# Optimization experiments

Hardware: AMD Instinct MI355X
Metric: run time of the kernel (lower is better)

The kernel has to match this reference:

```python
import jax, jax.numpy as jnp
import numpy as np

D_MODEL = 2048
N_HEADS = 16
HEAD_DIM = 128
ROPE_THETA = 10000.0


def _rope_cache(seq_len, dim, theta):
    inv_freq = 1.0 / (theta ** (jnp.arange(0, dim, 2, dtype=jnp.float32) / dim))
    t = jnp.arange(seq_len, dtype=jnp.float32)
    freqs = jnp.outer(t, inv_freq)          # [T, dim/2]
    emb = jnp.concatenate([freqs, freqs], axis=-1)  # [T, dim]
    return jnp.cos(emb), jnp.sin(emb)


def _rotate_half(x):
    d = x.shape[-1] // 2
    return jnp.concatenate([-x[..., d:], x[..., :d]], axis=-1)


def setup_inputs() -> dict:
    key = jax.random.key(0)
    k1, k2, k3 = jax.random.split(key, 3)
    B, T, D = 2, 2048, D_MODEL
    x = jax.random.normal(k1, (B, T, D), dtype=jnp.float32)
    w_qkv = jax.random.normal(k2, (D, 3 * D), dtype=jnp.float32) * (D ** -0.5)
    w_out = jax.random.normal(k3, (D, D), dtype=jnp.float32) * (D ** -0.5)
    return {"x": x, "w_qkv": w_qkv, "w_out": w_out}


def reference(x, w_qkv, w_out):
    B, T, D = x.shape
    H, Hd = N_HEADS, HEAD_DIM
    qkv = x @ w_qkv                                  # [B, T, 3D]
    q, k, v = jnp.split(qkv, 3, axis=-1)
    # [B, H, T, Hd]
    q = q.reshape(B, T, H, Hd).transpose(0, 2, 1, 3)
    k = k.reshape(B, T, H, Hd).transpose(0, 2, 1, 3)
    v = v.reshape(B, T, H, Hd).transpose(0, 2, 1, 3)
    cos, sin = _rope_cache(T, Hd, ROPE_THETA)        # [T, Hd]
    cos = cos[None, None]                            # [1,1,T,Hd]
    sin = sin[None, None]
    q = q * cos + _rotate_half(q) * sin
    k = k * cos + _rotate_half(k) * sin
    scale = Hd ** -0.5
    logits = jnp.einsum('bhqd,bhkd->bhqk', q, k) * scale
    causal = jnp.tril(jnp.ones((T, T), dtype=bool))
    logits = jnp.where(causal[None, None], logits, jnp.finfo(logits.dtype).min)
    attn = jax.nn.softmax(logits, axis=-1)
    out = jnp.einsum('bhqk,bhkd->bhqd', attn, v)     # [B,H,T,Hd]
    out = out.transpose(0, 2, 1, 3).reshape(B, T, D)
    return out @ w_out
```

## Files before the change

kernel.cpp:

```cpp
#include <hip/hip_runtime.h>

typedef unsigned short u16;
typedef unsigned int u32;
typedef __bf16 bf16x8 __attribute__((ext_vector_type(8)));
typedef float f32x4 __attribute__((ext_vector_type(4)));
typedef u16 u16x8 __attribute__((ext_vector_type(8)));

#define T_SEQ 2048
#define DMODEL 2048
#define NQKV 6144
#define HD 128
#define NH 16
#define MROWS 4096

__device__ __forceinline__ u16 f2b(float f) {
  union { float f; u32 u; } a; a.f = f;
  u32 r = a.u + 0x7fffu + ((a.u >> 16) & 1u);
  return (u16)(r >> 16);
}
__device__ __forceinline__ float b2f(u16 h) {
  union { u32 u; float f; } a; a.u = ((u32)h) << 16;
  return a.f;
}
__device__ __forceinline__ void g2l16(const u16* g, u16* l) {
  __builtin_amdgcn_global_load_lds((const __attribute__((address_space(1))) u32*)g,
                                   (__attribute__((address_space(3))) u32*)l, 16, 0, 0);
}

__global__ void k_f32_to_bf16(const float* __restrict__ in, u16* __restrict__ out, int n) {
  int i = (blockIdx.x * 256 + threadIdx.x) * 8;
  if (i >= n) return;
  float4 a = *(const float4*)(in + i);
  float4 b = *(const float4*)(in + i + 4);
  u16x8 v;
  v[0] = f2b(a.x); v[1] = f2b(a.y); v[2] = f2b(a.z); v[3] = f2b(a.w);
  v[4] = f2b(b.x); v[5] = f2b(b.y); v[6] = f2b(b.z); v[7] = f2b(b.w);
  *(u16x8*)(out + i) = v;
}

__global__ void k_transpose_bf16(const float* __restrict__ in, u16* __restrict__ out,
                                 int R, int C) {
  __shared__ u16 tile[32][33];
  const int c0 = blockIdx.x * 32, r0 = blockIdx.y * 32;
  const int tx = threadIdx.x & 31, ty = threadIdx.x >> 5;
#pragma unroll
  for (int i = 0; i < 32; i += 8)
    tile[ty + i][tx] = f2b(in[(size_t)(r0 + ty + i) * C + c0 + tx]);
  __syncthreads();
#pragma unroll
  for (int i = 0; i < 32; i += 8)
    out[(size_t)(c0 + ty + i) * R + r0 + tx] = tile[tx][ty + i];
}

__global__ void k_rope_cache(float* __restrict__ cosb, float* __restrict__ sinb) {
  int idx = blockIdx.x * 256 + threadIdx.x;
  int t = idx >> 6, d = idx & 63;
  float inv = powf(10000.0f, -(float)d * (1.0f / 64.0f));
  float fr = (float)t * inv;
  cosb[idx] = cosf(fr);
  sinb[idx] = sinf(fr);
}

template <int EPI>
__global__ __launch_bounds__(256) void k_gemm_nt(const u16* __restrict__ A,
                                                 const u16* __restrict__ B,
                                                 void* __restrict__ Cv,
                                                 int M, int N, int K) {
  __shared__ __align__(16) u16 lA[128 * 64];
  __shared__ __align__(16) u16 lB[128 * 64];
  const int tid = threadIdx.x;
  const int wid = tid >> 6, lane = tid & 63;
  const int g = lane >> 4, q = lane & 15;
  const int wr = wid >> 1, wc = wid & 1;
  const int bn = blockIdx.x, bm = blockIdx.y;
  const int l8 = lane >> 3, l7 = lane & 7;
  const f32x4 fzero = {0.f, 0.f, 0.f, 0.f};
  f32x4 acc[4][4];
#pragma unroll
  for (int m = 0; m < 4; ++m)
#pragma unroll
    for (int n = 0; n < 4; ++n) acc[m][n] = fzero;

  const u16* Ab = A + (size_t)bm * 128 * K;
  const u16* Bb = B + (size_t)bn * 128 * K;

  for (int k0 = 0; k0 < K; k0 += 64) {
    __syncthreads();
#pragma unroll
    for (int i = 0; i < 4; ++i) {
      int chunk = wid * 4 + i;
      int row = chunk * 8 + l8;
      int scol = (l7 * 8) ^ ((row & 7) << 3);
      g2l16(Ab + (size_t)row * K + k0 + scol, lA + chunk * 512);
      g2l16(Bb + (size_t)row * K + k0 + scol, lB + chunk * 512);
    }
    __syncthreads();
#pragma unroll
    for (int kk = 0; kk < 2; ++kk) {
      bf16x8 af[4], bfr[4];
#pragma unroll
      for (int m = 0; m < 4; ++m) {
        int row = wr * 64 + m * 16 + q;
        int col = (kk * 32 + g * 8) ^ ((row & 7) << 3);
        af[m] = *(const bf16x8*)(lA + row * 64 + col);
      }
#pragma unroll
      for (int n = 0; n < 4; ++n) {
        int row = wc * 64 + n * 16 + q;
        int col = (kk * 32 + g * 8) ^ ((row & 7) << 3);
        bfr[n] = *(const bf16x8*)(lB + row * 64 + col);
      }
#pragma unroll
      for (int m = 0; m < 4; ++m)
#pragma unroll
        for (int n = 0; n < 4; ++n)
          acc[m][n] = __builtin_amdgcn_mfma_f32_16x16x32_bf16(af[m], bfr[n], acc[m][n], 0, 0, 0);
    }
  }
  const int rbase = bm * 128 + wr * 64;
  const int cbase = bn * 128 + wc * 64;
#pragma unroll
  for (int m = 0; m < 4; ++m)
#pragma unroll
    for (int n = 0; n < 4; ++n) {
      int col = cbase + n * 16 + q;
#pragma unroll
      for (int r = 0; r < 4; ++r) {
        int row = rbase + m * 16 + g * 4 + r;
        if (EPI == 0)
          ((u16*)Cv)[(size_t)row * N + col] = f2b(acc[m][n][r]);
        else
          ((float*)Cv)[(size_t)row * N + col] = acc[m][n][r];
      }
    }
}

__global__ __launch_bounds__(256) void k_scatter_rope(const u16* __restrict__ qkv,
                                                      const float* __restrict__ cosb,
                                                      const float* __restrict__ sinb,
                                                      u16* __restrict__ qr,
                                                      u16* __restrict__ kr,
                                                      u16* __restrict__ vtb) {
  __shared__ __align__(16) u16 vtile[128][72];
  const int bh = blockIdx.x, b = bh >> 4, h = bh & 15;
  const int t0 = blockIdx.y * 64;
  const int tid = threadIdx.x;
  const float qscale = 0.08838834764831845f;
#pragma unroll
  for (int which = 0; which < 2; ++which) {
    u16* dst = which ? kr : qr;
    const int colbase = which * DMODEL + h * HD;
    const float sc = which ? 1.0f : qscale;
    for (int i = 0; i < 4; ++i) {
      int c = i * 256 + tid;
      int tt = c >> 4, d0 = (c & 15) * 8;
      int t = t0 + tt;
      size_t rowoff = (size_t)(b * T_SEQ + t) * NQKV + colbase;
      u16x8 xa = *(const u16x8*)(qkv + rowoff + d0);
      u16x8 xpart = *(const u16x8*)(qkv + rowoff + (d0 ^ 64));
      int dm = d0 & 63;
      bool lowhalf = d0 < 64;
      u16x8 y;
#pragma unroll
      for (int j = 0; j < 8; ++j) {
        float cv = cosb[t * 64 + dm + j];
        float sv = sinb[t * 64 + dm + j];
        float x0 = b2f(xa[j]), x1 = b2f(xpart[j]);
        float yv = lowhalf ? (x0 * cv - x1 * sv) : (x0 * cv + x1 * sv);
        y[j] = f2b(yv * sc);
      }
      *(u16x8*)(dst + ((size_t)bh * T_SEQ + t) * HD + d0) = y;
    }
  }
  for (int i = 0; i < 4; ++i) {
    int c = i * 256 + tid;
    int tt = c >> 4, d0 = (c & 15) * 8;
    size_t rowoff = (size_t)(b * T_SEQ + t0 + tt) * NQKV + 2 * DMODEL + h * HD;
    u16x8 xv = *(const u16x8*)(qkv + rowoff + d0);
#pragma unroll
    for (int j = 0; j < 8; ++j) vtile[d0 + j][tt] = xv[j];
  }
  __syncthreads();
  for (int i = 0; i < 4; ++i) {
    int c = i * 256 + tid;
    int d = c >> 3, tc = (c & 7) * 8;
    u16x8 y = *(const u16x8*)(&vtile[d][tc]);
    *(u16x8*)(vtb + ((size_t)bh * HD + d) * T_SEQ + t0 + tc) = y;
  }
}

__global__ __launch_bounds__(256) void k_attn(const u16* __restrict__ qr,
                                              const u16* __restrict__ kr,
                                              const u16* __restrict__ vtb,
                                              u16* __restrict__ ao) {
  __shared__ __align__(16) u16 lK[64 * 128];
  __shared__ __align__(16) u16 lV[128 * 64];
  __shared__ __align__(16) u16 lP[4][16 * 72];
  const int bh = blockIdx.x, b = bh >> 4, h = bh & 15;
  const int qt = blockIdx.y;
  const int tid = threadIdx.x;
  const int wid = tid >> 6, lane = tid & 63;
  const int g = lane >> 4, q = lane & 15;
  const int qw0 = qt * 64 + wid * 16;
  const u16* qb = qr + (size_t)bh * T_SEQ * HD;
  const u16* kbp = kr + (size_t)bh * T_SEQ * HD;
  const u16* vb = vtb + (size_t)bh * HD * T_SEQ;
  const f32x4 fzero = {0.f, 0.f, 0.f, 0.f};

  bf16x8 qf[4];
#pragma unroll
  for (int ks = 0; ks < 4; ++ks)
    qf[ks] = *(const bf16x8*)(qb + (size_t)(qw0 + q) * HD + ks * 32 + g * 8);

  f32x4 o_acc[8];
#pragma unroll
  for (int n = 0; n < 8; ++n) o_acc[n] = fzero;
  float m_run = -1e30f, l_run = 0.f;

  const int ntiles = qt + 1;
  for (int kt = 0; kt < ntiles; ++kt) {
    const int kb = kt * 64;
    __syncthreads();
#pragma unroll
    for (int i = 0; i < 4; ++i) {
      int chunk = wid * 4 + i;
      int row = chunk * 4 + g;
      int scol = (q * 8) ^ ((row & 7) << 3);
      g2l16(kbp + (size_t)(kb + row) * HD + scol, lK + chunk * 512);
    }
#pragma unroll
    for (int i = 0; i < 4; ++i) {
      int chunk = wid * 4 + i;
      int row = chunk * 8 + (lane >> 3);
      int scol = ((lane & 7) * 8) ^ ((row & 7) << 3);
      g2l16(vb + (size_t)row * T_SEQ + kb + scol, lV + chunk * 512);
    }
    __syncthreads();
    {
      f32x4 st[4];
#pragma unroll
      for (int m = 0; m < 4; ++m) st[m] = fzero;
#pragma unroll
      for (int ks = 0; ks < 4; ++ks) {
#pragma unroll
        for (int m = 0; m < 4; ++m) {
          int row = m * 16 + q;
          int col = (ks * 32 + g * 8) ^ ((row & 7) << 3);
          bf16x8 kf = *(const bf16x8*)(lK + row * 128 + col);
          st[m] = __builtin_amdgcn_mfma_f32_16x16x32_bf16(kf, qf[ks], st[m], 0, 0, 0);
        }
      }
      const int qrow = qw0 + q;
      float p[4][4];
      float pmax = -1e30f;
#pragma unroll
      for (int m = 0; m < 4; ++m)
#pragma unroll
        for (int r = 0; r < 4; ++r) {
          int kcol = kb + m * 16 + g * 4 + r;
          float s = (kcol <= qrow) ? st[m][r] : -1e30f;
          p[m][r] = s;
          pmax = fmaxf(pmax, s);
        }
      pmax = fmaxf(pmax, __shfl_xor(pmax, 16));
      pmax = fmaxf(pmax, __shfl_xor(pmax, 32));
      float m_new = fmaxf(m_run, pmax);
      float corr = __expf(m_run - m_new);
      float ls = 0.f;
#pragma unroll
      for (int m = 0; m < 4; ++m)
#pragma unroll
        for (int r = 0; r < 4; ++r) {
          float e = __expf(p[m][r] - m_new);
          p[m][r] = e;
          ls += e;
        }
      ls += __shfl_xor(ls, 16);
      ls += __shfl_xor(ls, 32);
      l_run = l_run * corr + ls;
      m_run = m_new;
#pragma unroll
      for (int m = 0; m < 4; ++m) {
#pragma unroll
        for (int rp = 0; rp < 2; ++rp) {
          u32 pk = (u32)f2b(p[m][rp * 2]) | ((u32)f2b(p[m][rp * 2 + 1]) << 16);
          *(u32*)(&lP[wid][q * 72 + m * 16 + g * 4 + rp * 2]) = pk;
        }
      }
      asm volatile("s_waitcnt lgkmcnt(0)" ::: "memory");
      __builtin_amdgcn_sched_barrier(0);
      float corr4[4];
#pragma unroll
      for (int r = 0; r < 4; ++r) corr4[r] = __shfl(corr, g * 4 + r);
#pragma unroll
      for (int n = 0; n < 8; ++n) {
#pragma unroll
        for (int r = 0; r < 4; ++r) o_acc[n][r] *= corr4[r];
      }
#pragma unroll
      for (int ks = 0; ks < 2; ++ks) {
        bf16x8 pf = *(const bf16x8*)(&lP[wid][q * 72 + ks * 32 + g * 8]);
#pragma unroll
        for (int n = 0; n < 8; ++n) {
          int row = n * 16 + q;
          int col = (ks * 32 + g * 8) ^ ((row & 7) << 3);
          bf16x8 vf = *(const bf16x8*)(lV + row * 64 + col);
          o_acc[n] = __builtin_amdgcn_mfma_f32_16x16x32_bf16(pf, vf, o_acc[n], 0, 0, 0);
        }
      }
    }
  }
  float linv[4];
#pragma unroll
  for (int r = 0; r < 4; ++r) {
    float lv = __shfl(l_run, g * 4 + r);
    linv[r] = 1.0f / lv;
  }
#pragma unroll
  for (int n = 0; n < 8; ++n)
#pragma unroll
    for (int r = 0; r < 4; ++r) {
      int trow = qw0 + g * 4 + r;
      ao[(size_t)(b * T_SEQ + trow) * DMODEL + h * HD + n * 16 + q] = f2b(o_acc[n][r] * linv[r]);
    }
}

extern "C" void kernel_launch(void* const* d_in, const int* in_sizes, int n_in,
                              void* d_out, int out_size, void* d_ws, size_t ws_size,
                              hipStream_t stream) {
  const float* x = (const float*)d_in[0];
  const float* w_qkv = (const float*)d_in[1];
  const float* w_out = (const float*)d_in[2];
  char* ws = (char*)d_ws;
  size_t off = 0;
  u16* xb = (u16*)(ws + off);    off += (size_t)MROWS * DMODEL * 2;
  u16* wqkvT = (u16*)(ws + off); off += (size_t)NQKV * DMODEL * 2;
  u16* woutT = (u16*)(ws + off); off += (size_t)DMODEL * DMODEL * 2;
  u16* qkv = (u16*)(ws + off);   off += (size_t)MROWS * NQKV * 2;
  u16* qr = (u16*)(ws + off);    off += (size_t)32 * T_SEQ * HD * 2;
  u16* kr = (u16*)(ws + off);    off += (size_t)32 * T_SEQ * HD * 2;
  u16* vtb = (u16*)(ws + off);   off += (size_t)32 * T_SEQ * HD * 2;
  float* cosb = (float*)(ws + off); off += (size_t)T_SEQ * 64 * 4;
  float* sinb = (float*)(ws + off); off += (size_t)T_SEQ * 64 * 4;
  u16* ao = xb;

  k_f32_to_bf16<<<dim3(MROWS * DMODEL / (256 * 8)), 256, 0, stream>>>(x, xb, MROWS * DMODEL);
  k_transpose_bf16<<<dim3(NQKV / 32, DMODEL / 32), 256, 0, stream>>>(w_qkv, wqkvT, DMODEL, NQKV);
  k_transpose_bf16<<<dim3(DMODEL / 32, DMODEL / 32), 256, 0, stream>>>(w_out, woutT, DMODEL, DMODEL);
  k_rope_cache<<<dim3(T_SEQ * 64 / 256), 256, 0, stream>>>(cosb, sinb);
  k_gemm_nt<0><<<dim3(NQKV / 128, MROWS / 128), 256, 0, stream>>>(xb, wqkvT, qkv, MROWS, NQKV, DMODEL);
  k_scatter_rope<<<dim3(32, T_SEQ / 64), 256, 0, stream>>>(qkv, cosb, sinb, qr, kr, vtb);
  k_attn<<<dim3(32, T_SEQ / 64), 256, 0, stream>>>(qr, kr, vtb, ao);
  k_gemm_nt<1><<<dim3(DMODEL / 128, MROWS / 128), 256, 0, stream>>>(ao, woutT, d_out, MROWS, DMODEL, DMODEL);
}
```

Before: 300.2 us.

## Replace GEMM with 8-wave 256-row tiled kernel using quarter-tile pipelined staging

Replaces the simple 128x128 single-buffered GEMM with an 8-wave (512-thread) kernel on 256xBN tiles. The kernel double-buffers LDS, splits each tile into half-tiles and interleaves async global-to-LDS loads for later k-tiles with MFMA phases, using explicit vmcnt waits, barriers and setprio. The goal is to hide global memory latency and raise arithmetic intensity for both the QKV and output projections. In exchange it uses more LDS, more registers and more complex synchronisation, and the larger tiles produce fewer blocks for the smaller output GEMM.

```diff
diff --git a/kernel.cpp b/kernel.cpp
--- a/kernel.cpp
+++ b/kernel.cpp
@@ -26,6 +26,8 @@
   __builtin_amdgcn_global_load_lds((const __attribute__((address_space(1))) u32*)g,
                                    (__attribute__((address_space(3))) u32*)l, 16, 0, 0);
 }
+
+#define BAR() do { asm volatile("" ::: "memory"); __builtin_amdgcn_s_barrier(); asm volatile("" ::: "memory"); } while (0)
 
 __global__ void k_f32_to_bf16(const float* __restrict__ in, u16* __restrict__ out, int n) {
   int i = (blockIdx.x * 256 + threadIdx.x) * 8;
@@ -61,78 +63,141 @@
   sinb[idx] = sinf(fr);
 }
 
-template <int EPI>
-__global__ __launch_bounds__(256) void k_gemm_nt(const u16* __restrict__ A,
-                                                 const u16* __restrict__ B,
-                                                 void* __restrict__ Cv,
-                                                 int M, int N, int K) {
-  __shared__ __align__(16) u16 lA[128 * 64];
-  __shared__ __align__(16) u16 lB[128 * 64];
+template <int BN, int EPI>
+__global__ __launch_bounds__(512, 2) void k_gemm8(const u16* __restrict__ A,
+                                                  const u16* __restrict__ B,
+                                                  void* __restrict__ Cv,
+                                                  int M, int N, int K) {
+  constexpr int HN = BN / 2;
+  constexpr int CW = BN / 8;
+  constexpr int FN = CW / 16;
+  constexpr int LB = (HN * 64 * 2) / (512 * 16);
+  constexpr int VM = LB + 2;
+
+  __shared__ __align__(16) u16 lA[2][2][128 * 64];
+  __shared__ __align__(16) u16 lB[2][2][HN * 64];
+
   const int tid = threadIdx.x;
   const int wid = tid >> 6, lane = tid & 63;
   const int g = lane >> 4, q = lane & 15;
-  const int wr = wid >> 1, wc = wid & 1;
-  const int bn = blockIdx.x, bm = blockIdx.y;
+  const int wm = wid >> 2, wn = wid & 3;
   const int l8 = lane >> 3, l7 = lane & 7;
+  const int bmBase = blockIdx.y * 256;
+  const int bnBase = blockIdx.x * BN;
+  const int NT = K >> 6;
+
   const f32x4 fzero = {0.f, 0.f, 0.f, 0.f};
-  f32x4 acc[4][4];
-#pragma unroll
-  for (int m = 0; m < 4; ++m)
-#pragma unroll
-    for (int n = 0; n < 4; ++n) acc[m][n] = fzero;
-
-  const u16* Ab = A + (size_t)bm * 128 * K;
-  const u16* Bb = B + (size_t)bn * 128 * K;
-
-  for (int k0 = 0; k0 < K; k0 += 64) {
-    __syncthreads();
-#pragma unroll
-    for (int i = 0; i < 4; ++i) {
-      int chunk = wid * 4 + i;
-      int row = chunk * 8 + l8;
-      int scol = (l7 * 8) ^ ((row & 7) << 3);
-      g2l16(Ab + (size_t)row * K + k0 + scol, lA + chunk * 512);
-      g2l16(Bb + (size_t)row * K + k0 + scol, lB + chunk * 512);
-    }
-    __syncthreads();
-#pragma unroll
-    for (int kk = 0; kk < 2; ++kk) {
-      bf16x8 af[4], bfr[4];
-#pragma unroll
-      for (int m = 0; m < 4; ++m) {
-        int row = wr * 64 + m * 16 + q;
-        int col = (kk * 32 + g * 8) ^ ((row & 7) << 3);
-        af[m] = *(const bf16x8*)(lA + row * 64 + col);
-      }
-#pragma unroll
-      for (int n = 0; n < 4; ++n) {
-        int row = wc * 64 + n * 16 + q;
-        int col = (kk * 32 + g * 8) ^ ((row & 7) << 3);
-        bfr[n] = *(const bf16x8*)(lB + row * 64 + col);
-      }
-#pragma unroll
-      for (int m = 0; m < 4; ++m)
-#pragma unroll
-        for (int n = 0; n < 4; ++n)
-          acc[m][n] = __builtin_amdgcn_mfma_f32_16x16x32_bf16(af[m], bfr[n], acc[m][n], 0, 0, 0);
-    }
-  }
-  const int rbase = bm * 128 + wr * 64;
-  const int cbase = bn * 128 + wc * 64;
-#pragma unroll
-  for (int m = 0; m < 4; ++m)
-#pragma unroll
-    for (int n = 0; n < 4; ++n) {
-      int col = cbase + n * 16 + q;
-#pragma unroll
-      for (int r = 0; r < 4; ++r) {
-        int row = rbase + m * 16 + g * 4 + r;
-        if (EPI == 0)
-          ((u16*)Cv)[(size_t)row * N + col] = f2b(acc[m][n][r]);
-        else
-          ((float*)Cv)[(size_t)row * N + col] = acc[m][n][r];
-      }
-    }
+  f32x4 acc[2][2][4][FN];
+#pragma unroll
+  for (int ha = 0; ha < 2; ++ha)
+#pragma unroll
+    for (int hb = 0; hb < 2; ++hb)
+#pragma unroll
+      for (int fm = 0; fm < 4; ++fm)
+#pragma unroll
+        for (int fn = 0; fn < FN; ++fn) acc[ha][hb][fm][fn] = fzero;
+
+  auto stageA = [&](int tile, int half, int bufI) {
+    if (tile < NT) {
+#pragma unroll
+      for (int j = 0; j < 2; ++j) {
+        int ch = wid * 2 + j;
+        int r = ch * 8 + l8;
+        int sc = (l7 * 8) ^ ((r & 7) << 3);
+        g2l16(A + (size_t)(bmBase + half * 128 + r) * K + (size_t)tile * 64 + sc,
+              &lA[bufI][half][ch * 512]);
+      }
+    }
+  };
+  auto stageB = [&](int tile, int half, int bufI) {
+    if (tile < NT) {
+#pragma unroll
+      for (int j = 0; j < LB; ++j) {
+        int ch = wid * LB + j;
+        int r = ch * 8 + l8;
+        int sc = (l7 * 8) ^ ((r & 7) << 3);
+        g2l16(B + (size_t)(bnBase + half * HN + r) * K + (size_t)tile * 64 + sc,
+              &lB[bufI][half][ch * 512]);
+      }
+    }
+  };
+
+  stageB(0, 0, 0); stageA(0, 1, 0); stageB(0, 1, 0); stageA(0, 0, 0);
+  stageB(1, 0, 1); stageA(1, 1, 1);
+  if constexpr (VM == 4) asm volatile("s_waitcnt vmcnt(4)" ::: "memory");
+  else                   asm volatile("s_waitcnt vmcnt(3)" ::: "memory");
+  BAR();
+
+#define PHASE(HA, HB, STAGE_STMT, WAIT_STMT)                                         \
+  do {                                                                               \
+    bf16x8 af[4][2];                                                                 \
+    bf16x8 bfr[FN][2];                                                               \
+    _Pragma("unroll") for (int fm = 0; fm < 4; ++fm) {                               \
+      int r = wm * 64 + fm * 16 + q;                                                 \
+      _Pragma("unroll") for (int kk = 0; kk < 2; ++kk) {                             \
+        int c = (kk * 32 + g * 8) ^ ((r & 7) << 3);                                  \
+        af[fm][kk] = *(const bf16x8*)&lA[buf][HA][r * 64 + c];                       \
+      }                                                                              \
+    }                                                                                \
+    _Pragma("unroll") for (int fn = 0; fn < FN; ++fn) {                              \
+      int r = wn * CW + fn * 16 + q;                                                 \
+      _Pragma("unroll") for (int kk = 0; kk < 2; ++kk) {                             \
+        int c = (kk * 32 + g * 8) ^ ((r & 7) << 3);                                  \
+        bfr[fn][kk] = *(const bf16x8*)&lB[buf][HB][r * 64 + c];                      \
+      }                                                                              \
+    }                                                                                \
+    STAGE_STMT;                                                                      \
+    WAIT_STMT;                                                                       \
+    BAR();                                                                           \
+    asm volatile("s_waitcnt lgkmcnt(0)" ::: "memory");                               \
+    __builtin_amdgcn_sched_barrier(0);                                               \
+    __builtin_amdgcn_s_setprio(1);                                                   \
+    _Pragma("unroll") for (int fm = 0; fm < 4; ++fm)                                 \
+      _Pragma("unroll") for (int fn = 0; fn < FN; ++fn) {                            \
+        acc[HA][HB][fm][fn] = __builtin_amdgcn_mfma_f32_16x16x32_bf16(               \
+            af[fm][0], bfr[fn][0], acc[HA][HB][fm][fn], 0, 0, 0);                    \
+        acc[HA][HB][fm][fn] = __builtin_amdgcn_mfma_f32_16x16x32_bf16(               \
+            af[fm][1], bfr[fn][1], acc[HA][HB][fm][fn], 0, 0, 0);                    \
+      }                                                                              \
+    __builtin_amdgcn_s_setprio(0);                                                   \
+    asm volatile("" ::: "memory");                                                   \
+    __builtin_amdgcn_s_barrier();                                                    \
+    asm volatile("" ::: "memory");                                                   \
+  } while (0)
+
+  for (int t = 0; t < NT; ++t) {
+    const int buf = t & 1;
+    PHASE(0, 0, stageB(t + 1, 1, buf ^ 1), );
+    PHASE(1, 0, stageA(t + 1, 0, buf ^ 1), );
+    PHASE(1, 1, stageB(t + 2, 0, buf), );
+    PHASE(0, 1, stageA(t + 2, 1, buf),
+          if (t + 2 < NT) {
+            if constexpr (VM == 4) asm volatile("s_waitcnt vmcnt(4)" ::: "memory");
+            else                   asm volatile("s_waitcnt vmcnt(3)" ::: "memory");
+          } else {
+            asm volatile("s_waitcnt vmcnt(0)" ::: "memory");
+          });
+  }
+#undef PHASE
+
+#pragma unroll
+  for (int ha = 0; ha < 2; ++ha)
+#pragma unroll
+    for (int hb = 0; hb < 2; ++hb)
+#pragma unroll
+      for (int fm = 0; fm < 4; ++fm)
+#pragma unroll
+        for (int fn = 0; fn < FN; ++fn) {
+          int col = bnBase + hb * HN + wn * CW + fn * 16 + q;
+#pragma unroll
+          for (int r = 0; r < 4; ++r) {
+            int row = bmBase + ha * 128 + wm * 64 + fm * 16 + g * 4 + r;
+            if (EPI == 0)
+              ((u16*)Cv)[(size_t)row * N + col] = f2b(acc[ha][hb][fm][fn][r]);
+            else
+              ((float*)Cv)[(size_t)row * N + col] = acc[ha][hb][fm][fn][r];
+          }
+        }
 }
 
 __global__ __launch_bounds__(256) void k_scatter_rope(const u16* __restrict__ qkv,
@@ -348,8 +413,8 @@
   k_transpose_bf16<<<dim3(NQKV / 32, DMODEL / 32), 256, 0, stream>>>(w_qkv, wqkvT, DMODEL, NQKV);
   k_transpose_bf16<<<dim3(DMODEL / 32, DMODEL / 32), 256, 0, stream>>>(w_out, woutT, DMODEL, DMODEL);
   k_rope_cache<<<dim3(T_SEQ * 64 / 256), 256, 0, stream>>>(cosb, sinb);
-  k_gemm_nt<0><<<dim3(NQKV / 128, MROWS / 128), 256, 0, stream>>>(xb, wqkvT, qkv, MROWS, NQKV, DMODEL);
+  k_gemm8<256, 0><<<dim3(NQKV / 256, MROWS / 256), 512, 0, stream>>>(xb, wqkvT, qkv, MROWS, NQKV, DMODEL);
   k_scatter_rope<<<dim3(32, T_SEQ / 64), 256, 0, stream>>>(qkv, cosb, sinb, qr, kr, vtb);
   k_attn<<<dim3(32, T_SEQ / 64), 256, 0, stream>>>(qr, kr, vtb, ao);
-  k_gemm_nt<1><<<dim3(DMODEL / 128, MROWS / 128), 256, 0, stream>>>(ao, woutT, d_out, MROWS, DMODEL, DMODEL);
-}
+  k_gemm8<128, 1><<<dim3(DMODEL / 128, MROWS / 256), 512, 0, stream>>>(ao, woutT, d_out, MROWS, DMODEL, DMODEL);
+}
```

Result: slower. 327.8 us (+9.2%).

## Use 256x256 eight-wave pipelined GEMM for QKV and reverse attention tile order

Applied to the files above, without the earlier changes.

Adds a new QKV projection GEMM with 512 threads and a 256x256 output tile. It uses double-buffered, XOR-swizzled LDS quadrants loaded via global_load_lds and interleaves staging, barriers and MFMA phases with raised priority. This aims to raise reuse and overlap memory with compute. Attention blocks now process query tiles in reverse order, so the longest causal tiles launch first for better load balance. The cost is heavy LDS use (128KB) and a fragile schedule built on waitcnt and barriers.

```diff
diff --git a/kernel.cpp b/kernel.cpp
--- a/kernel.cpp
+++ b/kernel.cpp
@@ -26,6 +26,8 @@
   __builtin_amdgcn_global_load_lds((const __attribute__((address_space(1))) u32*)g,
                                    (__attribute__((address_space(3))) u32*)l, 16, 0, 0);
 }
+
+#define BAR() do { asm volatile("" ::: "memory"); __builtin_amdgcn_s_barrier(); asm volatile("" ::: "memory"); } while (0)
 
 __global__ void k_f32_to_bf16(const float* __restrict__ in, u16* __restrict__ out, int n) {
   int i = (blockIdx.x * 256 + threadIdx.x) * 8;
@@ -59,6 +61,144 @@
   float fr = (float)t * inv;
   cosb[idx] = cosf(fr);
   sinb[idx] = sinf(fr);
+}
+
+template <int EPI>
+__global__ __launch_bounds__(512, 2) void k_gemm8(const u16* __restrict__ A,
+                                                  const u16* __restrict__ B,
+                                                  void* __restrict__ Cv,
+                                                  int M, int N, int K) {
+  __shared__ __align__(16) u16 lA[2][2][128 * 64];
+  __shared__ __align__(16) u16 lB[2][2][128 * 64];
+
+  const int tid = threadIdx.x;
+  const int wid = tid >> 6, lane = tid & 63;
+  const int g = lane >> 4, q = lane & 15;
+  const int wm = wid >> 2, wn = wid & 3;
+  const int l8 = lane >> 3, l7 = lane & 7;
+  const int bmBase = blockIdx.y * 256;
+  const int bnBase = blockIdx.x * 256;
+  const int NT = K >> 6;
+
+  const f32x4 fzero = {0.f, 0.f, 0.f, 0.f};
+  f32x4 acc[2][2][4][2];
+#pragma unroll
+  for (int ha = 0; ha < 2; ++ha)
+#pragma unroll
+    for (int hb = 0; hb < 2; ++hb)
+#pragma unroll
+      for (int fm = 0; fm < 4; ++fm)
+#pragma unroll
+        for (int fn = 0; fn < 2; ++fn) acc[ha][hb][fm][fn] = fzero;
+
+  auto stageA = [&](int tile, int half, int bufI) {
+    if (tile < NT) {
+#pragma unroll
+      for (int j = 0; j < 2; ++j) {
+        int ch = wid * 2 + j;
+        int r = ch * 8 + l8;
+        int sc = (l7 * 8) ^ ((r & 7) << 3);
+        g2l16(A + (size_t)(bmBase + half * 128 + r) * K + (size_t)tile * 64 + sc,
+              &lA[bufI][half][ch * 512]);
+      }
+    }
+  };
+  auto stageB = [&](int tile, int half, int bufI) {
+    if (tile < NT) {
+#pragma unroll
+      for (int j = 0; j < 2; ++j) {
+        int ch = wid * 2 + j;
+        int r = ch * 8 + l8;
+        int sc = (l7 * 8) ^ ((r & 7) << 3);
+        g2l16(B + (size_t)(bnBase + half * 128 + r) * K + (size_t)tile * 64 + sc,
+              &lB[bufI][half][ch * 512]);
+      }
+    }
+  };
+
+  bf16x8 aE[8], aO[8], bF[4];
+
+#define READ_A(dst, HA)                                                              \
+  _Pragma("unroll") for (int fm = 0; fm < 4; ++fm) {                                 \
+    int r = wm * 64 + fm * 16 + q;                                                   \
+    _Pragma("unroll") for (int kk = 0; kk < 2; ++kk) {                               \
+      int c = (kk * 32 + g * 8) ^ ((r & 7) << 3);                                    \
+      dst[fm * 2 + kk] = *(const bf16x8*)&lA[buf][HA][r * 64 + c];                   \
+    }                                                                                \
+  }
+#define READ_B(HB)                                                                   \
+  _Pragma("unroll") for (int fn = 0; fn < 2; ++fn) {                                 \
+    int r = wn * 32 + fn * 16 + q;                                                   \
+    _Pragma("unroll") for (int kk = 0; kk < 2; ++kk) {                               \
+      int c = (kk * 32 + g * 8) ^ ((r & 7) << 3);                                    \
+      bF[fn * 2 + kk] = *(const bf16x8*)&lB[buf][HB][r * 64 + c];                    \
+    }                                                                                \
+  }
+#define MFMA_Q(HA, HB, asrc)                                                         \
+  __builtin_amdgcn_s_setprio(1);                                                     \
+  _Pragma("unroll") for (int fm = 0; fm < 4; ++fm)                                   \
+    _Pragma("unroll") for (int fn = 0; fn < 2; ++fn) {                               \
+      acc[HA][HB][fm][fn] = __builtin_amdgcn_mfma_f32_16x16x32_bf16(                 \
+          asrc[fm * 2 + 0], bF[fn * 2 + 0], acc[HA][HB][fm][fn], 0, 0, 0);           \
+      acc[HA][HB][fm][fn] = __builtin_amdgcn_mfma_f32_16x16x32_bf16(                 \
+          asrc[fm * 2 + 1], bF[fn * 2 + 1], acc[HA][HB][fm][fn], 0, 0, 0);           \
+    }                                                                                \
+  __builtin_amdgcn_s_setprio(0);
+#define LGKM0() do { asm volatile("s_waitcnt lgkmcnt(0)" ::: "memory"); \
+                     __builtin_amdgcn_sched_barrier(0); } while (0)
+
+  stageB(0, 0, 0); stageA(0, 0, 0); stageA(0, 1, 0); stageB(0, 1, 0);
+  stageB(1, 0, 1); stageA(1, 1, 1);
+  asm volatile("s_waitcnt vmcnt(4)" ::: "memory");
+  BAR();
+
+  for (int t = 0; t < NT; ++t) {
+    const int buf = t & 1;
+    READ_A(aE, 0); READ_B(0);
+    stageB(t + 1, 1, buf ^ 1);
+    BAR(); LGKM0();
+    MFMA_Q(0, 0, aE);
+    BAR();
+    READ_A(aO, 1);
+    stageA(t + 1, 0, buf ^ 1);
+    BAR(); LGKM0();
+    MFMA_Q(1, 0, aO);
+    BAR();
+    READ_B(1);
+    stageB(t + 2, 0, buf);
+    BAR(); LGKM0();
+    MFMA_Q(1, 1, aO);
+    BAR();
+    stageA(t + 2, 1, buf);
+    if (t + 2 < NT) asm volatile("s_waitcnt vmcnt(4)" ::: "memory");
+    else            asm volatile("s_waitcnt vmcnt(0)" ::: "memory");
+    BAR();
+    MFMA_Q(0, 1, aE);
+    BAR();
+  }
+#undef READ_A
+#undef READ_B
+#undef MFMA_Q
+#undef LGKM0
+
+#pragma unroll
+  for (int ha = 0; ha < 2; ++ha)
+#pragma unroll
+    for (int hb = 0; hb < 2; ++hb)
+#pragma unroll
+      for (int fm = 0; fm < 4; ++fm)
+#pragma unroll
+        for (int fn = 0; fn < 2; ++fn) {
+          int col = bnBase + hb * 128 + wn * 32 + fn * 16 + q;
+#pragma unroll
+          for (int r = 0; r < 4; ++r) {
+            int row = bmBase + ha * 128 + wm * 64 + fm * 16 + g * 4 + r;
+            if (EPI == 0)
+              ((u16*)Cv)[(size_t)row * N + col] = f2b(acc[ha][hb][fm][fn][r]);
+            else
+              ((float*)Cv)[(size_t)row * N + col] = acc[ha][hb][fm][fn][r];
+          }
+        }
 }
 
 template <int EPI>
@@ -197,7 +337,7 @@
   __shared__ __align__(16) u16 lV[128 * 64];
   __shared__ __align__(16) u16 lP[4][16 * 72];
   const int bh = blockIdx.x, b = bh >> 4, h = bh & 15;
-  const int qt = blockIdx.y;
+  const int qt = (T_SEQ / 64 - 1) - blockIdx.y;
   const int tid = threadIdx.x;
   const int wid = tid >> 6, lane = tid & 63;
   const int g = lane >> 4, q = lane & 15;
@@ -348,7 +488,7 @@
   k_transpose_bf16<<<dim3(NQKV / 32, DMODEL / 32), 256, 0, stream>>>(w_qkv, wqkvT, DMODEL, NQKV);
   k_transpose_bf16<<<dim3(DMODEL / 32, DMODEL / 32), 256, 0, stream>>>(w_out, woutT, DMODEL, DMODEL);
   k_rope_cache<<<dim3(T_SEQ * 64 / 256), 256, 0, stream>>>(cosb, sinb);
-  k_gemm_nt<0><<<dim3(NQKV / 128, MROWS / 128), 256, 0, stream>>>(xb, wqkvT, qkv, MROWS, NQKV, DMODEL);
+  k_gemm8<0><<<dim3(NQKV / 256, MROWS / 256), 512, 0, stream>>>(xb, wqkvT, qkv, MROWS, NQKV, DMODEL);
   k_scatter_rope<<<dim3(32, T_SEQ / 64), 256, 0, stream>>>(qkv, cosb, sinb, qr, kr, vtb);
   k_attn<<<dim3(32, T_SEQ / 64), 256, 0, stream>>>(qr, kr, vtb, ao);
   k_gemm_nt<1><<<dim3(DMODEL / 128, MROWS / 128), 256, 0, stream>>>(ao, woutT, d_out, MROWS, DMODEL, DMODEL);
```

Result: faster. 282.5 us (-5.9%).

## Fuse RoPE and head scatter into QKV GEMM epilogue; reverse attention tile order

Applied to the files above, without the earlier changes.

Adds a QKV GEMM whose epilogue applies RoPE and writes q, k and transposed v directly in head-major layout. The wave column mapping is rearranged so each wave holds both rotary halves of a head. This removes the intermediate qkv buffer and the separate scatter kernel, saving a full write and read of that tensor. Attention blocks are also launched in reverse query-tile order so the heaviest causal tiles start first. In exchange, the epilogue does scalar 2-byte stores with strided layouts, which may coalesce poorly.

```diff
diff --git a/kernel.cpp b/kernel.cpp
--- a/kernel.cpp
+++ b/kernel.cpp
@@ -4,6 +4,7 @@
 typedef unsigned int u32;
 typedef __bf16 bf16x8 __attribute__((ext_vector_type(8)));
 typedef float f32x4 __attribute__((ext_vector_type(4)));
+typedef u16 u16x4 __attribute__((ext_vector_type(4)));
 typedef u16 u16x8 __attribute__((ext_vector_type(8)));
 
 #define T_SEQ 2048
@@ -59,6 +60,108 @@
   float fr = (float)t * inv;
   cosb[idx] = cosf(fr);
   sinb[idx] = sinf(fr);
+}
+
+__global__ __launch_bounds__(256) void k_gemm_qkv(const u16* __restrict__ A,
+                                                  const u16* __restrict__ B,
+                                                  const float* __restrict__ cosb,
+                                                  const float* __restrict__ sinb,
+                                                  u16* __restrict__ qr,
+                                                  u16* __restrict__ kr,
+                                                  u16* __restrict__ vtb) {
+  __shared__ __align__(16) u16 lA[128 * 64];
+  __shared__ __align__(16) u16 lB[128 * 64];
+  const int K = DMODEL;
+  const int tid = threadIdx.x;
+  const int wid = tid >> 6, lane = tid & 63;
+  const int g = lane >> 4, q = lane & 15;
+  const int wr = wid >> 1, wc = wid & 1;
+  const int bn = blockIdx.x, bm = blockIdx.y;
+  const int l8 = lane >> 3, l7 = lane & 7;
+  const f32x4 fzero = {0.f, 0.f, 0.f, 0.f};
+  f32x4 acc[4][4];
+#pragma unroll
+  for (int m = 0; m < 4; ++m)
+#pragma unroll
+    for (int n = 0; n < 4; ++n) acc[m][n] = fzero;
+
+  const u16* Ab = A + (size_t)bm * 128 * K;
+  const u16* Bb = B + (size_t)bn * 128 * K;
+
+  for (int k0 = 0; k0 < K; k0 += 64) {
+    __syncthreads();
+#pragma unroll
+    for (int i = 0; i < 4; ++i) {
+      int chunk = wid * 4 + i;
+      int row = chunk * 8 + l8;
+      int scol = (l7 * 8) ^ ((row & 7) << 3);
+      g2l16(Ab + (size_t)row * K + k0 + scol, lA + chunk * 512);
+      g2l16(Bb + (size_t)row * K + k0 + scol, lB + chunk * 512);
+    }
+    __syncthreads();
+#pragma unroll
+    for (int kk = 0; kk < 2; ++kk) {
+      bf16x8 af[4], bfr[4];
+#pragma unroll
+      for (int m = 0; m < 4; ++m) {
+        int row = wr * 64 + m * 16 + q;
+        int col = (kk * 32 + g * 8) ^ ((row & 7) << 3);
+        af[m] = *(const bf16x8*)(lA + row * 64 + col);
+      }
+#pragma unroll
+      for (int n = 0; n < 4; ++n) {
+        int row = wc * 32 + (n & 1) * 16 + (n >> 1) * 64 + q;
+        int col = (kk * 32 + g * 8) ^ ((row & 7) << 3);
+        bfr[n] = *(const bf16x8*)(lB + row * 64 + col);
+      }
+#pragma unroll
+      for (int m = 0; m < 4; ++m)
+#pragma unroll
+        for (int n = 0; n < 4; ++n)
+          acc[m][n] = __builtin_amdgcn_mfma_f32_16x16x32_bf16(af[m], bfr[n], acc[m][n], 0, 0, 0);
+    }
+  }
+
+  const int h = bn & 15;
+  const int which = bn >> 4;
+  const int b = bm >> 4;
+  const int bh = b * 16 + h;
+  const int tb0 = (bm & 15) * 128 + wr * 64;
+  const float qscale = 0.08838834764831845f;
+
+  if (which == 2) {
+    u16* vdst = vtb + (size_t)bh * HD * T_SEQ;
+#pragma unroll
+    for (int m = 0; m < 4; ++m)
+#pragma unroll
+      for (int n = 0; n < 4; ++n) {
+        int c = wc * 32 + (n & 1) * 16 + (n >> 1) * 64 + q;
+        int t0 = tb0 + m * 16 + g * 4;
+        u16x4 pk;
+#pragma unroll
+        for (int r = 0; r < 4; ++r) pk[r] = f2b(acc[m][n][r]);
+        *(u16x4*)(vdst + (size_t)c * T_SEQ + t0) = pk;
+      }
+  } else {
+    u16* dst = (which ? kr : qr) + (size_t)bh * T_SEQ * HD;
+    const float sc = which ? 1.0f : qscale;
+#pragma unroll
+    for (int m = 0; m < 4; ++m)
+#pragma unroll
+      for (int n = 0; n < 2; ++n) {
+        int dm = wc * 32 + n * 16 + q;
+#pragma unroll
+        for (int r = 0; r < 4; ++r) {
+          int t = tb0 + m * 16 + g * 4 + r;
+          float cv = cosb[t * 64 + dm];
+          float sv = sinb[t * 64 + dm];
+          float x0 = acc[m][n][r];
+          float x1 = acc[m][n + 2][r];
+          dst[(size_t)t * HD + dm] = f2b((x0 * cv - x1 * sv) * sc);
+          dst[(size_t)t * HD + 64 + dm] = f2b((x1 * cv + x0 * sv) * sc);
+        }
+      }
+  }
 }
 
 template <int EPI>
@@ -135,60 +238,6 @@
     }
 }
 
-__global__ __launch_bounds__(256) void k_scatter_rope(const u16* __restrict__ qkv,
-                                                      const float* __restrict__ cosb,
-                                                      const float* __restrict__ sinb,
-                                                      u16* __restrict__ qr,
-                                                      u16* __restrict__ kr,
-                                                      u16* __restrict__ vtb) {
-  __shared__ __align__(16) u16 vtile[128][72];
-  const int bh = blockIdx.x, b = bh >> 4, h = bh & 15;
-  const int t0 = blockIdx.y * 64;
-  const int tid = threadIdx.x;
-  const float qscale = 0.08838834764831845f;
-#pragma unroll
-  for (int which = 0; which < 2; ++which) {
-    u16* dst = which ? kr : qr;
-    const int colbase = which * DMODEL + h * HD;
-    const float sc = which ? 1.0f : qscale;
-    for (int i = 0; i < 4; ++i) {
-      int c = i * 256 + tid;
-      int tt = c >> 4, d0 = (c & 15) * 8;
-      int t = t0 + tt;
-      size_t rowoff = (size_t)(b * T_SEQ + t) * NQKV + colbase;
-      u16x8 xa = *(const u16x8*)(qkv + rowoff + d0);
-      u16x8 xpart = *(const u16x8*)(qkv + rowoff + (d0 ^ 64));
-      int dm = d0 & 63;
-      bool lowhalf = d0 < 64;
-      u16x8 y;
-#pragma unroll
-      for (int j = 0; j < 8; ++j) {
-        float cv = cosb[t * 64 + dm + j];
-        float sv = sinb[t * 64 + dm + j];
-        float x0 = b2f(xa[j]), x1 = b2f(xpart[j]);
-        float yv = lowhalf ? (x0 * cv - x1 * sv) : (x0 * cv + x1 * sv);
-        y[j] = f2b(yv * sc);
-      }
-      *(u16x8*)(dst + ((size_t)bh * T_SEQ + t) * HD + d0) = y;
-    }
-  }
-  for (int i = 0; i < 4; ++i) {
-    int c = i * 256 + tid;
-    int tt = c >> 4, d0 = (c & 15) * 8;
-    size_t rowoff = (size_t)(b * T_SEQ + t0 + tt) * NQKV + 2 * DMODEL + h * HD;
-    u16x8 xv = *(const u16x8*)(qkv + rowoff + d0);
-#pragma unroll
-    for (int j = 0; j < 8; ++j) vtile[d0 + j][tt] = xv[j];
-  }
-  __syncthreads();
-  for (int i = 0; i < 4; ++i) {
-    int c = i * 256 + tid;
-    int d = c >> 3, tc = (c & 7) * 8;
-    u16x8 y = *(const u16x8*)(&vtile[d][tc]);
-    *(u16x8*)(vtb + ((size_t)bh * HD + d) * T_SEQ + t0 + tc) = y;
-  }
-}
-
 __global__ __launch_bounds__(256) void k_attn(const u16* __restrict__ qr,
                                               const u16* __restrict__ kr,
                                               const u16* __restrict__ vtb,
@@ -197,7 +246,7 @@
   __shared__ __align__(16) u16 lV[128 * 64];
   __shared__ __align__(16) u16 lP[4][16 * 72];
   const int bh = blockIdx.x, b = bh >> 4, h = bh & 15;
-  const int qt = blockIdx.y;
+  const int qt = (T_SEQ / 64 - 1) - blockIdx.y;
   const int tid = threadIdx.x;
   const int wid = tid >> 6, lane = tid & 63;
   const int g = lane >> 4, q = lane & 15;
@@ -336,7 +385,6 @@
   u16* xb = (u16*)(ws + off);    off += (size_t)MROWS * DMODEL * 2;
   u16* wqkvT = (u16*)(ws + off); off += (size_t)NQKV * DMODEL * 2;
   u16* woutT = (u16*)(ws + off); off += (size_t)DMODEL * DMODEL * 2;
-  u16* qkv = (u16*)(ws + off);   off += (size_t)MROWS * NQKV * 2;
   u16* qr = (u16*)(ws + off);    off += (size_t)32 * T_SEQ * HD * 2;
   u16* kr = (u16*)(ws + off);    off += (size_t)32 * T_SEQ * HD * 2;
   u16* vtb = (u16*)(ws + off);   off += (size_t)32 * T_SEQ * HD * 2;
@@ -348,8 +396,7 @@
   k_transpose_bf16<<<dim3(NQKV / 32, DMODEL / 32), 256, 0, stream>>>(w_qkv, wqkvT, DMODEL, NQKV);
   k_transpose_bf16<<<dim3(DMODEL / 32, DMODEL / 32), 256, 0, stream>>>(w_out, woutT, DMODEL, DMODEL);
   k_rope_cache<<<dim3(T_SEQ * 64 / 256), 256, 0, stream>>>(cosb, sinb);
-  k_gemm_nt<0><<<dim3(NQKV / 128, MROWS / 128), 256, 0, stream>>>(xb, wqkvT, qkv, MROWS, NQKV, DMODEL);
-  k_scatter_rope<<<dim3(32, T_SEQ / 64), 256, 0, stream>>>(qkv, cosb, sinb, qr, kr, vtb);
+  k_gemm_qkv<<<dim3(NQKV / 128, MROWS / 128), 256, 0, stream>>>(xb, wqkvT, cosb, sinb, qr, kr, vtb);
   k_attn<<<dim3(32, T_SEQ / 64), 256, 0, stream>>>(qr, kr, vtb, ao);
   k_gemm_nt<1><<<dim3(DMODEL / 128, MROWS / 128), 256, 0, stream>>>(ao, woutT, d_out, MROWS, DMODEL, DMODEL);
 }
```

Measured after the change: 264.9 us. 11.8% less time.
